# Kernel optimization log

Hardware: AMD Instinct MI355X
Metric: run time of the kernel (lower is better)

## Reference

```python
import jax, jax.numpy as jnp
import numpy as np
import math

N, C3, T = 32, 192, 2048  # C3 = 3 * head_dim

def setup_inputs() -> dict:
    key = jax.random.key(0)
    qkv = jax.random.normal(key, (N, C3, T), dtype=jnp.float32)
    return {"qkv": qkv}

def reference(qkv):
    ch = qkv.shape[1] // 3
    q, k, v = jnp.split(qkv, 3, axis=1)              # each [N, C, T]
    scale = 1.0 / math.sqrt(math.sqrt(ch))           # applied to both q and k
    # [N, T, T] attention scores
    weight = jnp.einsum('bct,bcs->bts', q * scale, k * scale)
    weight = jax.nn.softmax(weight.astype(jnp.float32), axis=-1).astype(qkv.dtype)
    # [N, C, T] output
    return jnp.einsum('bts,bcs->bct', weight, v)
```

## Files before the change

### kernel.cpp

```cpp
#include <hip/hip_runtime.h>

#define T_DIM 2048
#define D_DIM 64
#define NB 32

#define QT_OFF 0
#define KB_OFF 4194304
#define VB_OFF 8388608

typedef _Float16 half8 __attribute__((ext_vector_type(8)));
typedef _Float16 half4 __attribute__((ext_vector_type(4)));
typedef float f32x16 __attribute__((ext_vector_type(16)));
typedef float f32x4 __attribute__((ext_vector_type(4)));

#define ZERO16 (f32x16){0.f,0.f,0.f,0.f,0.f,0.f,0.f,0.f,0.f,0.f,0.f,0.f,0.f,0.f,0.f,0.f}

__global__ __launch_bounds__(256) void prepass(const float* __restrict__ qkv,
                                               _Float16* __restrict__ ws) {
  const int ttile = blockIdx.x;
  const int b = blockIdx.y;
  const int type = blockIdx.z;
  const int t0 = ttile * 64;
  __shared__ float Ls[64][65];

  const int tid = threadIdx.x;
  const int cc = tid >> 4;
  const int tt = (tid & 15) << 2;
  const float QS = 0.125f * 1.4426950408889634f;
  const float* src = qkv + ((size_t)b * 192 + type * 64) * T_DIM;
#pragma unroll
  for (int p = 0; p < 4; ++p) {
    const int c = p * 16 + cc;
    float4 v = *(const float4*)&src[(size_t)c * T_DIM + t0 + tt];
    if (type == 0) { v.x *= QS; v.y *= QS; v.z *= QS; v.w *= QS; }
    Ls[c][tt] = v.x; Ls[c][tt + 1] = v.y; Ls[c][tt + 2] = v.z; Ls[c][tt + 3] = v.w;
  }
  __syncthreads();

  if (type == 0) {
    const int t = tid >> 2, cg = (tid & 3) * 16;
    half8 h0, h1;
#pragma unroll
    for (int j = 0; j < 8; ++j) h0[j] = (_Float16)Ls[cg + j][t];
#pragma unroll
    for (int j = 0; j < 8; ++j) h1[j] = (_Float16)Ls[cg + 8 + j][t];
    _Float16* dst = ws + QT_OFF + ((size_t)b * T_DIM + t0 + t) * 64 + cg;
    *(half8*)dst = h0;
    *(half8*)(dst + 8) = h1;
  } else if (type == 1) {
    const int f = tid >> 6, h = (tid >> 5) & 1, s31 = tid & 31;
#pragma unroll
    for (int sbl = 0; sbl < 2; ++sbl) {
      const int sb = (t0 >> 5) + sbl;
      half8 hv;
#pragma unroll
      for (int j = 0; j < 8; ++j) hv[j] = (_Float16)Ls[f * 16 + h * 8 + j][sbl * 32 + s31];
      _Float16* dst = ws + KB_OFF + ((size_t)b * 64 + sb) * 2048 + f * 512 + h * 256 + s31 * 8;
      *(half8*)dst = hv;
    }
  } else {
#pragma unroll
    for (int p = 0; p < 2; ++p) {
      const int g = p * 256 + tid;
      const int sgl = g >> 6, c = g & 63;
      half8 hv;
#pragma unroll
      for (int j = 0; j < 8; ++j) hv[j] = (_Float16)Ls[c][sgl * 8 + j];
      _Float16* dst = ws + VB_OFF + (((size_t)b * 256 + (t0 >> 3) + sgl) * 64 + c) * 8;
      *(half8*)dst = hv;
    }
  }
}

__global__ __launch_bounds__(256, 2) void qkv_main(const _Float16* __restrict__ ws,
                                                   float* __restrict__ out) {
  const int tid = threadIdx.x;
  const int wave = tid >> 6, lane = tid & 63;
  const int l31 = lane & 31, h = lane >> 5;
  const int b = blockIdx.x & 31;
  const int qg = blockIdx.x >> 5;
  const int t0 = qg * 128 + wave * 32;

  const _Float16* Qt = ws + QT_OFF;
  const _Float16* kbase = ws + KB_OFF + (size_t)b * 131072;
  const _Float16* vbase = ws + VB_OFF + (size_t)b * 131072;

  const _Float16* qp = Qt + ((size_t)b * T_DIM + t0 + l31) * 64 + h * 8;
  half8 bq[4];
#pragma unroll
  for (int f = 0; f < 4; ++f) bq[f] = *(const half8*)(qp + f * 16);

  f32x16 o0 = ZERO16, o1 = ZERO16;
  float lp = 0.f;

  const _Float16* kp = kbase + h * 256 + l31 * 8;
  const _Float16* vp = vbase + l31 * 8 + h * 4;

  half8 ak[4];
#pragma unroll
  for (int f = 0; f < 4; ++f) ak[f] = *(const half8*)(kp + f * 512);

  for (int sb = 0; sb < 64; ++sb) {
    const _Float16* kn = kp + (size_t)(sb + 1 < 64 ? sb + 1 : sb) * 2048;
    half8 an0 = *(const half8*)(kn);
    half8 an1 = *(const half8*)(kn + 512);
    half8 an2 = *(const half8*)(kn + 1024);
    half8 an3 = *(const half8*)(kn + 1536);

    f32x16 s = ZERO16;
    s = __builtin_amdgcn_mfma_f32_32x32x16_f16(ak[0], bq[0], s, 0, 0, 0);
    s = __builtin_amdgcn_mfma_f32_32x32x16_f16(ak[1], bq[1], s, 0, 0, 0);
    s = __builtin_amdgcn_mfma_f32_32x32x16_f16(ak[2], bq[2], s, 0, 0, 0);
    s = __builtin_amdgcn_mfma_f32_32x32x16_f16(ak[3], bq[3], s, 0, 0, 0);

    const _Float16* vpi = vp + (size_t)sb * 2048;
    half4 bv[8];
#pragma unroll
    for (int g = 0; g < 4; ++g) {
      bv[2 * g] = *(const half4*)(vpi + g * 512);
      bv[2 * g + 1] = *(const half4*)(vpi + g * 512 + 256);
    }

    half4 ap[4];
#pragma unroll
    for (int g = 0; g < 4; ++g) {
      const float e0 = __builtin_amdgcn_exp2f(s[4 * g + 0]);
      const float e1 = __builtin_amdgcn_exp2f(s[4 * g + 1]);
      const float e2 = __builtin_amdgcn_exp2f(s[4 * g + 2]);
      const float e3 = __builtin_amdgcn_exp2f(s[4 * g + 3]);
      lp += (e0 + e1) + (e2 + e3);
      ap[g] = (half4){(_Float16)e0, (_Float16)e1, (_Float16)e2, (_Float16)e3};
    }

#pragma unroll
    for (int g = 0; g < 4; ++g) {
      o0 = __builtin_amdgcn_mfma_f32_32x32x8f16(ap[g], bv[2 * g], o0, 0, 0, 0);
      o1 = __builtin_amdgcn_mfma_f32_32x32x8f16(ap[g], bv[2 * g + 1], o1, 0, 0, 0);
    }

    ak[0] = an0; ak[1] = an1; ak[2] = an2; ak[3] = an3;
  }

  const float lf = lp + __shfl_xor(lp, 32);
  const float linv = 1.0f / lf;
  float* ob = out + (size_t)b * D_DIM * T_DIM;
#pragma unroll
  for (int g = 0; g < 4; ++g) {
    f32x4 r0, r1;
#pragma unroll
    for (int j = 0; j < 4; ++j) {
      const float il = __shfl(linv, g * 8 + h * 4 + j);
      r0[j] = o0[g * 4 + j] * il;
      r1[j] = o1[g * 4 + j] * il;
    }
    const int q = t0 + g * 8 + h * 4;
    *(f32x4*)&ob[(size_t)l31 * T_DIM + q] = r0;
    *(f32x4*)&ob[(size_t)(32 + l31) * T_DIM + q] = r1;
  }
}

extern "C" void kernel_launch(void* const* d_in, const int* in_sizes, int n_in,
                              void* d_out, int out_size, void* d_ws, size_t ws_size,
                              hipStream_t stream) {
  const float* qkv = (const float*)d_in[0];
  float* out = (float*)d_out;
  _Float16* ws = (_Float16*)d_ws;
  hipLaunchKernelGGL(prepass, dim3(32, 32, 3), dim3(256), 0, stream, qkv, ws);
  hipLaunchKernelGGL(qkv_main, dim3(512), dim3(256), 0, stream, ws, out);
}
```

Baseline: 140.4 us.

## Switch attention to 16x16 MFMA tiles with doubled grid and rewritten prepass

Result: slower. 184.9 us (+31.7%).

```diff
diff --git a/kernel.cpp b/kernel.cpp
--- a/kernel.cpp
+++ b/kernel.cpp
@@ -1,7 +1,6 @@
 #include <hip/hip_runtime.h>
 
 #define T_DIM 2048
-#define D_DIM 64
 #define NB 32
 
 #define QT_OFF 0
@@ -10,153 +9,144 @@
 
 typedef _Float16 half8 __attribute__((ext_vector_type(8)));
 typedef _Float16 half4 __attribute__((ext_vector_type(4)));
-typedef float f32x16 __attribute__((ext_vector_type(16)));
 typedef float f32x4 __attribute__((ext_vector_type(4)));
-
-#define ZERO16 (f32x16){0.f,0.f,0.f,0.f,0.f,0.f,0.f,0.f,0.f,0.f,0.f,0.f,0.f,0.f,0.f,0.f}
 
 __global__ __launch_bounds__(256) void prepass(const float* __restrict__ qkv,
                                                _Float16* __restrict__ ws) {
-  const int ttile = blockIdx.x;
+  const int seg = blockIdx.x;
   const int b = blockIdx.y;
   const int type = blockIdx.z;
-  const int t0 = ttile * 64;
-  __shared__ float Ls[64][65];
+  const int tid = threadIdx.x;
+  const float* __restrict__ src = qkv + ((size_t)b * 192 + type * 64) * T_DIM;
 
-  const int tid = threadIdx.x;
-  const int cc = tid >> 4;
-  const int tt = (tid & 15) << 2;
-  const float QS = 0.125f * 1.4426950408889634f;
-  const float* src = qkv + ((size_t)b * 192 + type * 64) * T_DIM;
+  if (type < 2) {
+    const int tr = tid & 7;
+    const int cg = (tid >> 3) & 7;
+    const int wv = tid >> 6;
+    const float QS = (type == 0) ? 0.125f * 1.4426950408889634f : 1.0f;
+    _Float16* qdst = ws + QT_OFF + (size_t)b * T_DIM * 64 + cg * 8;
+    _Float16* kdst = ws + KB_OFF + (size_t)b * 131072 + (cg >> 1) * 512 + (cg & 1) * 256;
 #pragma unroll
-  for (int p = 0; p < 4; ++p) {
-    const int c = p * 16 + cc;
-    float4 v = *(const float4*)&src[(size_t)c * T_DIM + t0 + tt];
-    if (type == 0) { v.x *= QS; v.y *= QS; v.z *= QS; v.w *= QS; }
-    Ls[c][tt] = v.x; Ls[c][tt + 1] = v.y; Ls[c][tt + 2] = v.z; Ls[c][tt + 3] = v.w;
-  }
-  __syncthreads();
-
-  if (type == 0) {
-    const int t = tid >> 2, cg = (tid & 3) * 16;
-    half8 h0, h1;
+    for (int pass = 0; pass < 8; ++pass) {
+      const int t = seg * 256 + pass * 32 + wv * 8 + tr;
+      float f[8];
 #pragma unroll
-    for (int j = 0; j < 8; ++j) h0[j] = (_Float16)Ls[cg + j][t];
-#pragma unroll
-    for (int j = 0; j < 8; ++j) h1[j] = (_Float16)Ls[cg + 8 + j][t];
-    _Float16* dst = ws + QT_OFF + ((size_t)b * T_DIM + t0 + t) * 64 + cg;
-    *(half8*)dst = h0;
-    *(half8*)(dst + 8) = h1;
-  } else if (type == 1) {
-    const int f = tid >> 6, h = (tid >> 5) & 1, s31 = tid & 31;
-#pragma unroll
-    for (int sbl = 0; sbl < 2; ++sbl) {
-      const int sb = (t0 >> 5) + sbl;
+      for (int j = 0; j < 8; ++j) f[j] = src[(size_t)(cg * 8 + j) * T_DIM + t] * QS;
       half8 hv;
 #pragma unroll
-      for (int j = 0; j < 8; ++j) hv[j] = (_Float16)Ls[f * 16 + h * 8 + j][sbl * 32 + s31];
-      _Float16* dst = ws + KB_OFF + ((size_t)b * 64 + sb) * 2048 + f * 512 + h * 256 + s31 * 8;
-      *(half8*)dst = hv;
+      for (int j = 0; j < 8; ++j) hv[j] = (_Float16)f[j];
+      if (type == 0) {
+        *(half8*)(qdst + (size_t)t * 64) = hv;
+      } else {
+        *(half8*)(kdst + (size_t)(t >> 5) * 2048 + (t & 31) * 8) = hv;
+      }
     }
   } else {
+    const int c = tid & 63;
+    const int sq = tid >> 6;
+    _Float16* vdst = ws + VB_OFF + (size_t)b * 131072 + c * 8;
 #pragma unroll
-    for (int p = 0; p < 2; ++p) {
-      const int g = p * 256 + tid;
-      const int sgl = g >> 6, c = g & 63;
-      half8 hv;
-#pragma unroll
-      for (int j = 0; j < 8; ++j) hv[j] = (_Float16)Ls[c][sgl * 8 + j];
-      _Float16* dst = ws + VB_OFF + (((size_t)b * 256 + (t0 >> 3) + sgl) * 64 + c) * 8;
-      *(half8*)dst = hv;
+    for (int i = 0; i < 8; ++i) {
+      const int sg = seg * 32 + sq * 8 + i;
+      const float4 a = *(const float4*)&src[(size_t)c * T_DIM + sg * 8];
+      const float4 d = *(const float4*)&src[(size_t)c * T_DIM + sg * 8 + 4];
+      half8 hv = {(_Float16)a.x, (_Float16)a.y, (_Float16)a.z, (_Float16)a.w,
+                  (_Float16)d.x, (_Float16)d.y, (_Float16)d.z, (_Float16)d.w};
+      *(half8*)(vdst + (size_t)sg * 512) = hv;
     }
   }
 }
 
-__global__ __launch_bounds__(256, 2) void qkv_main(const _Float16* __restrict__ ws,
+__global__ __launch_bounds__(256, 4) void qkv_main(const _Float16* __restrict__ ws,
                                                    float* __restrict__ out) {
   const int tid = threadIdx.x;
   const int wave = tid >> 6, lane = tid & 63;
-  const int l31 = lane & 31, h = lane >> 5;
+  const int l15 = lane & 15, quad = lane >> 4;
   const int b = blockIdx.x & 31;
   const int qg = blockIdx.x >> 5;
-  const int t0 = qg * 128 + wave * 32;
+  const int t0 = qg * 64 + wave * 16;
 
-  const _Float16* Qt = ws + QT_OFF;
-  const _Float16* kbase = ws + KB_OFF + (size_t)b * 131072;
-  const _Float16* vbase = ws + VB_OFF + (size_t)b * 131072;
+  const _Float16* qp = ws + QT_OFF + ((size_t)b * T_DIM + t0 + l15) * 64 + quad * 8;
+  const half8 bq0 = *(const half8*)qp;
+  const half8 bq1 = *(const half8*)(qp + 32);
 
-  const _Float16* qp = Qt + ((size_t)b * T_DIM + t0 + l31) * 64 + h * 8;
-  half8 bq[4];
-#pragma unroll
-  for (int f = 0; f < 4; ++f) bq[f] = *(const half8*)(qp + f * 16);
+  const _Float16* kp = ws + KB_OFF + (size_t)b * 131072
+                       + (quad >> 1) * 512 + (quad & 1) * 256 + l15 * 8;
+  const _Float16* vp = ws + VB_OFF + (size_t)b * 131072
+                       + (quad >> 1) * 512 + l15 * 8 + (quad & 1) * 4;
 
-  f32x16 o0 = ZERO16, o1 = ZERO16;
+  f32x4 o0 = {0.f,0.f,0.f,0.f}, o1 = {0.f,0.f,0.f,0.f};
+  f32x4 o2 = {0.f,0.f,0.f,0.f}, o3 = {0.f,0.f,0.f,0.f};
   float lp = 0.f;
 
-  const _Float16* kp = kbase + h * 256 + l31 * 8;
-  const _Float16* vp = vbase + l31 * 8 + h * 4;
-
-  half8 ak[4];
-#pragma unroll
-  for (int f = 0; f < 4; ++f) ak[f] = *(const half8*)(kp + f * 512);
+  half8 ak00 = *(const half8*)(kp);
+  half8 ak01 = *(const half8*)(kp + 1024);
+  half8 ak10 = *(const half8*)(kp + 128);
+  half8 ak11 = *(const half8*)(kp + 1152);
+  half4 av00 = *(const half4*)(vp);
+  half4 av01 = *(const half4*)(vp + 1024);
+  half4 av10 = *(const half4*)(vp + 128);
+  half4 av11 = *(const half4*)(vp + 1152);
+  half4 av20 = *(const half4*)(vp + 256);
+  half4 av21 = *(const half4*)(vp + 1280);
+  half4 av30 = *(const half4*)(vp + 384);
+  half4 av31 = *(const half4*)(vp + 1408);
 
   for (int sb = 0; sb < 64; ++sb) {
-    const _Float16* kn = kp + (size_t)(sb + 1 < 64 ? sb + 1 : sb) * 2048;
-    half8 an0 = *(const half8*)(kn);
-    half8 an1 = *(const half8*)(kn + 512);
-    half8 an2 = *(const half8*)(kn + 1024);
-    half8 an3 = *(const half8*)(kn + 1536);
+    const size_t off = (size_t)(sb + 1 < 64 ? sb + 1 : sb) * 2048;
+    half8 nk00 = *(const half8*)(kp + off);
+    half8 nk01 = *(const half8*)(kp + off + 1024);
+    half8 nk10 = *(const half8*)(kp + off + 128);
+    half8 nk11 = *(const half8*)(kp + off + 1152);
+    half4 nv00 = *(const half4*)(vp + off);
+    half4 nv01 = *(const half4*)(vp + off + 1024);
+    half4 nv10 = *(const half4*)(vp + off + 128);
+    half4 nv11 = *(const half4*)(vp + off + 1152);
+    half4 nv20 = *(const half4*)(vp + off + 256);
+    half4 nv21 = *(const half4*)(vp + off + 1280);
+    half4 nv30 = *(const half4*)(vp + off + 384);
+    half4 nv31 = *(const half4*)(vp + off + 1408);
 
-    f32x16 s = ZERO16;
-    s = __builtin_amdgcn_mfma_f32_32x32x16_f16(ak[0], bq[0], s, 0, 0, 0);
-    s = __builtin_amdgcn_mfma_f32_32x32x16_f16(ak[1], bq[1], s, 0, 0, 0);
-    s = __builtin_amdgcn_mfma_f32_32x32x16_f16(ak[2], bq[2], s, 0, 0, 0);
-    s = __builtin_amdgcn_mfma_f32_32x32x16_f16(ak[3], bq[3], s, 0, 0, 0);
+    f32x4 s0 = {0.f,0.f,0.f,0.f}, s1 = {0.f,0.f,0.f,0.f};
+    s0 = __builtin_amdgcn_mfma_f32_16x16x32_f16(ak00, bq0, s0, 0, 0, 0);
+    s1 = __builtin_amdgcn_mfma_f32_16x16x32_f16(ak10, bq0, s1, 0, 0, 0);
+    s0 = __builtin_amdgcn_mfma_f32_16x16x32_f16(ak01, bq1, s0, 0, 0, 0);
+    s1 = __builtin_amdgcn_mfma_f32_16x16x32_f16(ak11, bq1, s1, 0, 0, 0);
 
-    const _Float16* vpi = vp + (size_t)sb * 2048;
-    half4 bv[8];
+    half4 ap0, ap1;
 #pragma unroll
-    for (int g = 0; g < 4; ++g) {
-      bv[2 * g] = *(const half4*)(vpi + g * 512);
-      bv[2 * g + 1] = *(const half4*)(vpi + g * 512 + 256);
+    for (int r = 0; r < 4; ++r) {
+      const float e0 = __builtin_amdgcn_exp2f(s0[r]);
+      const float e1 = __builtin_amdgcn_exp2f(s1[r]);
+      lp += e0 + e1;
+      ap0[r] = (_Float16)e0;
+      ap1[r] = (_Float16)e1;
     }
 
-    half4 ap[4];
-#pragma unroll
-    for (int g = 0; g < 4; ++g) {
-      const float e0 = __builtin_amdgcn_exp2f(s[4 * g + 0]);
-      const float e1 = __builtin_amdgcn_exp2f(s[4 * g + 1]);
-      const float e2 = __builtin_amdgcn_exp2f(s[4 * g + 2]);
-      const float e3 = __builtin_amdgcn_exp2f(s[4 * g + 3]);
-      lp += (e0 + e1) + (e2 + e3);
-      ap[g] = (half4){(_Float16)e0, (_Float16)e1, (_Float16)e2, (_Float16)e3};
-    }
+    o0 = __builtin_amdgcn_mfma_f32_16x16x16f16(av00, ap0, o0, 0, 0, 0);
+    o1 = __builtin_amdgcn_mfma_f32_16x16x16f16(av10, ap0, o1, 0, 0, 0);
+    o2 = __builtin_amdgcn_mfma_f32_16x16x16f16(av20, ap0, o2, 0, 0, 0);
+    o3 = __builtin_amdgcn_mfma_f32_16x16x16f16(av30, ap0, o3, 0, 0, 0);
+    o0 = __builtin_amdgcn_mfma_f32_16x16x16f16(av01, ap1, o0, 0, 0, 0);
+    o1 = __builtin_amdgcn_mfma_f32_16x16x16f16(av11, ap1, o1, 0, 0, 0);
+    o2 = __builtin_amdgcn_mfma_f32_16x16x16f16(av21, ap1, o2, 0, 0, 0);
+    o3 = __builtin_amdgcn_mfma_f32_16x16x16f16(av31, ap1, o3, 0, 0, 0);
 
-#pragma unroll
-    for (int g = 0; g < 4; ++g) {
-      o0 = __builtin_amdgcn_mfma_f32_32x32x8f16(ap[g], bv[2 * g], o0, 0, 0, 0);
-      o1 = __builtin_amdgcn_mfma_f32_32x32x8f16(ap[g], bv[2 * g + 1], o1, 0, 0, 0);
-    }
-
-    ak[0] = an0; ak[1] = an1; ak[2] = an2; ak[3] = an3;
+    ak00 = nk00; ak01 = nk01; ak10 = nk10; ak11 = nk11;
+    av00 = nv00; av01 = nv01; av10 = nv10; av11 = nv11;
+    av20 = nv20; av21 = nv21; av30 = nv30; av31 = nv31;
   }
 
-  const float lf = lp + __shfl_xor(lp, 32);
-  const float linv = 1.0f / lf;
-  float* ob = out + (size_t)b * D_DIM * T_DIM;
+  lp += __shfl_xor(lp, 16);
+  lp += __shfl_xor(lp, 32);
+  const float linv = 1.0f / lp;
+  float* ob = out + (size_t)b * 64 * T_DIM + t0 + l15;
+  f32x4 oo[4] = {o0, o1, o2, o3};
 #pragma unroll
-  for (int g = 0; g < 4; ++g) {
-    f32x4 r0, r1;
+  for (int ct = 0; ct < 4; ++ct)
 #pragma unroll
-    for (int j = 0; j < 4; ++j) {
-      const float il = __shfl(linv, g * 8 + h * 4 + j);
-      r0[j] = o0[g * 4 + j] * il;
-      r1[j] = o1[g * 4 + j] * il;
-    }
-    const int q = t0 + g * 8 + h * 4;
-    *(f32x4*)&ob[(size_t)l31 * T_DIM + q] = r0;
-    *(f32x4*)&ob[(size_t)(32 + l31) * T_DIM + q] = r1;
-  }
+    for (int r = 0; r < 4; ++r)
+      ob[(size_t)(ct * 16 + quad * 4 + r) * T_DIM] = oo[ct][r] * linv;
 }
 
 extern "C" void kernel_launch(void* const* d_in, const int* in_sizes, int n_in,
@@ -165,6 +155,6 @@
   const float* qkv = (const float*)d_in[0];
   float* out = (float*)d_out;
   _Float16* ws = (_Float16*)d_ws;
-  hipLaunchKernelGGL(prepass, dim3(32, 32, 3), dim3(256), 0, stream, qkv, ws);
-  hipLaunchKernelGGL(qkv_main, dim3(512), dim3(256), 0, stream, ws, out);
+  hipLaunchKernelGGL(prepass, dim3(8, 32, 3), dim3(256), 0, stream, qkv, ws);
+  hipLaunchKernelGGL(qkv_main, dim3(1024), dim3(256), 0, stream, ws, out);
 }
```

## Split key range across waves and combine partial outputs through shared memory

Applied to the files above, without the earlier changes.

Measured after the change: 141.5 us. About the same (+0.7%).

```diff
diff --git a/kernel.cpp b/kernel.cpp
--- a/kernel.cpp
+++ b/kernel.cpp
@@ -1,7 +1,6 @@
 #include <hip/hip_runtime.h>
 
 #define T_DIM 2048
-#define D_DIM 64
 #define NB 32
 
 #define QT_OFF 0
@@ -72,20 +71,23 @@
   }
 }
 
-__global__ __launch_bounds__(256, 2) void qkv_main(const _Float16* __restrict__ ws,
+__global__ __launch_bounds__(256, 4) void qkv_main(const _Float16* __restrict__ ws,
                                                    float* __restrict__ out) {
   const int tid = threadIdx.x;
   const int wave = tid >> 6, lane = tid & 63;
   const int l31 = lane & 31, h = lane >> 5;
+  const int qh = wave & 1;
+  const int kh = wave >> 1;
   const int b = blockIdx.x & 31;
   const int qg = blockIdx.x >> 5;
-  const int t0 = qg * 128 + wave * 32;
+  const int t0 = qg * 64 + qh * 32;
 
-  const _Float16* Qt = ws + QT_OFF;
-  const _Float16* kbase = ws + KB_OFF + (size_t)b * 131072;
-  const _Float16* vbase = ws + VB_OFF + (size_t)b * 131072;
+  __shared__ float cl[2][64][36];
 
-  const _Float16* qp = Qt + ((size_t)b * T_DIM + t0 + l31) * 64 + h * 8;
+  const _Float16* kbase = ws + KB_OFF + (size_t)b * 131072 + (size_t)kh * 65536;
+  const _Float16* vbase = ws + VB_OFF + (size_t)b * 131072 + (size_t)kh * 65536;
+
+  const _Float16* qp = ws + QT_OFF + ((size_t)b * T_DIM + t0 + l31) * 64 + h * 8;
   half8 bq[4];
 #pragma unroll
   for (int f = 0; f < 4; ++f) bq[f] = *(const half8*)(qp + f * 16);
@@ -96,23 +98,17 @@
   const _Float16* kp = kbase + h * 256 + l31 * 8;
   const _Float16* vp = vbase + l31 * 8 + h * 4;
 
-  half8 ak[4];
-#pragma unroll
-  for (int f = 0; f < 4; ++f) ak[f] = *(const half8*)(kp + f * 512);
+  half8 ak0 = *(const half8*)(kp);
+  half8 ak1 = *(const half8*)(kp + 512);
+  half8 ak2 = *(const half8*)(kp + 1024);
+  half8 ak3 = *(const half8*)(kp + 1536);
 
-  for (int sb = 0; sb < 64; ++sb) {
-    const _Float16* kn = kp + (size_t)(sb + 1 < 64 ? sb + 1 : sb) * 2048;
-    half8 an0 = *(const half8*)(kn);
-    half8 an1 = *(const half8*)(kn + 512);
-    half8 an2 = *(const half8*)(kn + 1024);
-    half8 an3 = *(const half8*)(kn + 1536);
-
-    f32x16 s = ZERO16;
-    s = __builtin_amdgcn_mfma_f32_32x32x16_f16(ak[0], bq[0], s, 0, 0, 0);
-    s = __builtin_amdgcn_mfma_f32_32x32x16_f16(ak[1], bq[1], s, 0, 0, 0);
-    s = __builtin_amdgcn_mfma_f32_32x32x16_f16(ak[2], bq[2], s, 0, 0, 0);
-    s = __builtin_amdgcn_mfma_f32_32x32x16_f16(ak[3], bq[3], s, 0, 0, 0);
-
+  for (int sb = 0; sb < 32; ++sb) {
+    const size_t off = (size_t)(sb + 1 < 32 ? sb + 1 : sb) * 2048;
+    half8 nk0 = *(const half8*)(kp + off);
+    half8 nk1 = *(const half8*)(kp + off + 512);
+    half8 nk2 = *(const half8*)(kp + off + 1024);
+    half8 nk3 = *(const half8*)(kp + off + 1536);
     const _Float16* vpi = vp + (size_t)sb * 2048;
     half4 bv[8];
 #pragma unroll
@@ -121,16 +117,25 @@
       bv[2 * g + 1] = *(const half4*)(vpi + g * 512 + 256);
     }
 
+    f32x16 s = ZERO16;
+    s = __builtin_amdgcn_mfma_f32_32x32x16_f16(ak0, bq[0], s, 0, 0, 0);
+    s = __builtin_amdgcn_mfma_f32_32x32x16_f16(ak1, bq[1], s, 0, 0, 0);
+    s = __builtin_amdgcn_mfma_f32_32x32x16_f16(ak2, bq[2], s, 0, 0, 0);
+    s = __builtin_amdgcn_mfma_f32_32x32x16_f16(ak3, bq[3], s, 0, 0, 0);
+
     half4 ap[4];
+    float lp0 = 0.f, lp1 = 0.f;
 #pragma unroll
     for (int g = 0; g < 4; ++g) {
       const float e0 = __builtin_amdgcn_exp2f(s[4 * g + 0]);
       const float e1 = __builtin_amdgcn_exp2f(s[4 * g + 1]);
       const float e2 = __builtin_amdgcn_exp2f(s[4 * g + 2]);
       const float e3 = __builtin_amdgcn_exp2f(s[4 * g + 3]);
-      lp += (e0 + e1) + (e2 + e3);
+      lp0 += e0 + e1;
+      lp1 += e2 + e3;
       ap[g] = (half4){(_Float16)e0, (_Float16)e1, (_Float16)e2, (_Float16)e3};
     }
+    lp += lp0 + lp1;
 
 #pragma unroll
     for (int g = 0; g < 4; ++g) {
@@ -138,24 +143,48 @@
       o1 = __builtin_amdgcn_mfma_f32_32x32x8f16(ap[g], bv[2 * g + 1], o1, 0, 0, 0);
     }
 
-    ak[0] = an0; ak[1] = an1; ak[2] = an2; ak[3] = an3;
+    ak0 = nk0; ak1 = nk1; ak2 = nk2; ak3 = nk3;
   }
 
-  const float lf = lp + __shfl_xor(lp, 32);
-  const float linv = 1.0f / lf;
-  float* ob = out + (size_t)b * D_DIM * T_DIM;
+  if (kh == 1) {
 #pragma unroll
-  for (int g = 0; g < 4; ++g) {
-    f32x4 r0, r1;
+    for (int g = 0; g < 4; ++g) {
+      *(f32x4*)&cl[qh][lane][g * 4] =
+          (f32x4){o0[4 * g], o0[4 * g + 1], o0[4 * g + 2], o0[4 * g + 3]};
+      *(f32x4*)&cl[qh][lane][16 + g * 4] =
+          (f32x4){o1[4 * g], o1[4 * g + 1], o1[4 * g + 2], o1[4 * g + 3]};
+    }
+    cl[qh][lane][32] = lp;
+  }
+  __syncthreads();
+  if (kh == 0) {
 #pragma unroll
-    for (int j = 0; j < 4; ++j) {
-      const float il = __shfl(linv, g * 8 + h * 4 + j);
-      r0[j] = o0[g * 4 + j] * il;
-      r1[j] = o1[g * 4 + j] * il;
+    for (int g = 0; g < 4; ++g) {
+      const f32x4 p0 = *(const f32x4*)&cl[qh][lane][g * 4];
+      const f32x4 p1 = *(const f32x4*)&cl[qh][lane][16 + g * 4];
+#pragma unroll
+      for (int j = 0; j < 4; ++j) {
+        o0[4 * g + j] += p0[j];
+        o1[4 * g + j] += p1[j];
+      }
     }
-    const int q = t0 + g * 8 + h * 4;
-    *(f32x4*)&ob[(size_t)l31 * T_DIM + q] = r0;
-    *(f32x4*)&ob[(size_t)(32 + l31) * T_DIM + q] = r1;
+    lp += cl[qh][lane][32];
+    const float lf = lp + __shfl_xor(lp, 32);
+    const float linv = 1.0f / lf;
+    float* ob = out + (size_t)b * 64 * T_DIM + t0;
+#pragma unroll
+    for (int g = 0; g < 4; ++g) {
+      f32x4 r0, r1;
+#pragma unroll
+      for (int j = 0; j < 4; ++j) {
+        const float il = __shfl(linv, g * 8 + h * 4 + j);
+        r0[j] = o0[g * 4 + j] * il;
+        r1[j] = o1[g * 4 + j] * il;
+      }
+      const int q = g * 8 + h * 4;
+      *(f32x4*)&ob[(size_t)l31 * T_DIM + q] = r0;
+      *(f32x4*)&ob[(size_t)(32 + l31) * T_DIM + q] = r1;
+    }
   }
 }
 
@@ -166,5 +195,5 @@
   float* out = (float*)d_out;
   _Float16* ws = (_Float16*)d_ws;
   hipLaunchKernelGGL(prepass, dim3(32, 32, 3), dim3(256), 0, stream, qkv, ws);
-  hipLaunchKernelGGL(qkv_main, dim3(512), dim3(256), 0, stream, ws, out);
+  hipLaunchKernelGGL(qkv_main, dim3(1024), dim3(256), 0, stream, ws, out);
 }
```
